# Performance work log

Hardware: AMD Instinct MI355X
Metric: run time of the kernel (lower is better)

Reference implementation:

```python
import jax, jax.numpy as jnp
import numpy as np

B, L, D_SEQ, D_GLOBAL = 32, 2048, 1024, 1024
H, DK, DV = 16, 64, 64


def setup_inputs() -> dict:
    key = jax.random.key(0)
    k1, k2, k3, k4, k5 = jax.random.split(key, 5)
    scale = 0.05
    return {
        "X": jax.random.normal(k1, (B, D_GLOBAL), dtype=jnp.float32),
        "S": jax.random.normal(k2, (B, L, D_SEQ), dtype=jnp.float32),
        "Wq": jax.random.normal(k3, (H, D_GLOBAL, DK), dtype=jnp.float32) * scale,
        "Wk": jax.random.normal(k4, (H, D_SEQ, DK), dtype=jnp.float32) * scale,
        "Wv": jax.random.normal(k5, (H, D_SEQ, DV), dtype=jnp.float32) * scale,
    }


def reference(X, S, Wq, Wk, Wv):
    # X: [B, d_global], S: [B, L, d_seq]
    d_key = Wq.shape[-1]
    inv_sqrt_dk = 1.0 / jnp.sqrt(jnp.float32(d_key))
    # Values: gelu (exact, erf-based like tf default) projection -> [B, H, L, DV]
    VS = jax.nn.gelu(jnp.einsum("bld,hdv->bhlv", S, Wv), approximate=False)
    # Single global query per head: tanh projection -> [B, H, DK]
    Q = jnp.tanh(jnp.einsum("bd,hdk->bhk", X, Wq))
    # Keys: tanh projection -> [B, H, L, DK]
    KS = jnp.tanh(jnp.einsum("bld,hdk->bhlk", S, Wk))
    # Attention logits (batched GEMV): [B, H, L]
    logits = jnp.einsum("bhk,bhlk->bhl", Q, KS) * inv_sqrt_dk
    Z = jax.nn.softmax(logits, axis=-1)
    # Weighted sum of values: [B, H, DV] -> flatten to [B, H*DV]
    Y = jnp.einsum("bhl,bhlv->bhv", Z, VS)
    return Y.reshape(Y.shape[0], -1)
```

## Files before the change

### kernel.cpp

```cpp
#include <hip/hip_runtime.h>
#include <math.h>

#define B_   32
#define L_   2048
#define DSEQ 1024
#define DGLB 1024
#define H_   16
#define DK_  64
#define DV_  64
#define LT   64
#define NT   (L_/LT)
#define PSTRIDE 66

#define WC_KSTRIDE 4096
#define WC_HSTRIDE 131072

#define AS1 __attribute__((address_space(1)))
#define AS3 __attribute__((address_space(3)))

using u16    = unsigned short;
using bf16x8 = __attribute__((ext_vector_type(8))) short;
using f32x4  = __attribute__((ext_vector_type(4))) float;

__device__ __forceinline__ u16 f2bf(float x) {
  union { float f; unsigned int u; } v; v.f = x;
  return (u16)((v.u + 0x7fffu + ((v.u >> 16) & 1u)) >> 16);
}

__device__ __forceinline__ float tanh_fast(float x) {
  float e = __builtin_exp2f(x * 2.885390081777927f);
  return 1.f - 2.f/(e + 1.f);
}

__device__ __forceinline__ float erf_fast(float x) {
  float ax = fabsf(x);
  float t  = 1.f/(1.f + 0.3275911f*ax);
  float p  = t*(0.254829592f + t*(-0.284496736f + t*(1.421413741f +
             t*(-1.453152027f + t*1.061405429f))));
  float e  = __builtin_exp2f(-ax*ax*1.4426950408889634f);
  float r  = 1.f - p*e;
  return copysignf(r, x);
}

#define PHASE_BARRIER(N)                                   \
  do {                                                     \
    __builtin_amdgcn_sched_barrier(0);                     \
    asm volatile("s_waitcnt vmcnt(" #N ")" ::: "memory");  \
    __builtin_amdgcn_s_barrier();                          \
    __builtin_amdgcn_sched_barrier(0);                     \
  } while (0)

__global__ void pack_w_kernel(const float* __restrict__ Wk,
                              const float* __restrict__ Wv,
                              u16* __restrict__ Wc) {
  const int h = blockIdx.x, j = blockIdx.y;
  const float* src = (j < DK_) ? (Wk + (size_t)h*DSEQ*DK_ + j)
                               : (Wv + (size_t)h*DSEQ*DV_ + (j - DK_));
  u16* dst = Wc + (size_t)h*WC_HSTRIDE + (size_t)j*32;
  for (int d = threadIdx.x; d < DSEQ; d += blockDim.x)
    dst[(size_t)(d >> 5)*WC_KSTRIDE + (d & 31)] = f2bf(src[(size_t)d*64]);
}

__global__ void s2bf_kernel(const float* __restrict__ S, u16* __restrict__ Sb) {
  const size_t G = (size_t)B_*L_*DSEQ/8;
  for (size_t i = (size_t)blockIdx.x*256 + threadIdx.x; i < G; i += (size_t)4096*256) {
    const float4* sp = (const float4*)(S + i*8);
    float4 v0 = sp[0], v1 = sp[1];
    bf16x8 wv;
    wv[0]=(short)f2bf(v0.x); wv[1]=(short)f2bf(v0.y);
    wv[2]=(short)f2bf(v0.z); wv[3]=(short)f2bf(v0.w);
    wv[4]=(short)f2bf(v1.x); wv[5]=(short)f2bf(v1.y);
    wv[6]=(short)f2bf(v1.z); wv[7]=(short)f2bf(v1.w);
    *(bf16x8*)(Sb + i*8) = wv;
  }
}

__global__ void q_proj_kernel(const float* __restrict__ X,
                              const float* __restrict__ Wq,
                              float* __restrict__ Q) {
  const int h = blockIdx.x, b0 = blockIdx.y*4, k = threadIdx.x;
  const float* w = Wq + (size_t)h*DGLB*DK_ + k;
  float a0=0.f, a1=0.f, a2=0.f, a3=0.f;
  for (int d = 0; d < DGLB; ++d) {
    float wv = w[(size_t)d*DK_];
    a0 += X[(size_t)(b0+0)*DGLB + d]*wv;
    a1 += X[(size_t)(b0+1)*DGLB + d]*wv;
    a2 += X[(size_t)(b0+2)*DGLB + d]*wv;
    a3 += X[(size_t)(b0+3)*DGLB + d]*wv;
  }
  Q[((size_t)(b0+0)*H_+h)*DK_+k] = tanhf(a0);
  Q[((size_t)(b0+1)*H_+h)*DK_+k] = tanhf(a1);
  Q[((size_t)(b0+2)*H_+h)*DK_+k] = tanhf(a2);
  Q[((size_t)(b0+3)*H_+h)*DK_+k] = tanhf(a3);
}

template<int BF16SRC>
__global__ __launch_bounds__(256, 3) void fused_kernel(
    const float* __restrict__ S, const u16* __restrict__ Sb,
    const u16* __restrict__ Wc, const float* __restrict__ Q,
    float* __restrict__ part) {
  __shared__ u16   Slds[3*64*128];
  __shared__ float lpart[2][64];

  const int id   = blockIdx.x;
  const int slot = id & 7;
  const int m    = id >> 3;
  const int tile = (m + (slot << 7)) & 1023;
  const int t    = tile & (NT-1), b = tile >> 5;

  const int tid  = threadIdx.x;
  const int wave = tid >> 6, lane = tid & 63;
  const int lhi  = lane >> 4, llo = lane & 15;
  const int isV  = wave & 1,  hp  = wave >> 1;
  const int h    = slot*2 + hp;

  const u16* wb = Wc + (size_t)h*WC_HSTRIDE + (size_t)(isV*64 + llo)*32 + lhi*8;
  int arow[4];
  #pragma unroll
  for (int rt = 0; rt < 4; ++rt) arow[rt] = (rt*16 + llo)*256;

  const u16*   Sv = Sb + ((size_t)b*L_ + (size_t)t*LT)*DSEQ;
  const float* Sf = S  + ((size_t)b*L_ + (size_t)t*LT)*DSEQ;

  auto stage_gl = [&](int sub) {
    const int bs = (sub % 3) * 8192;
    #pragma unroll
    for (int it = 0; it < 4; ++it) {
      const int j   = wave*4 + it;
      const int row = 4*j + (lane >> 4);
      const int g   = (lane & 15) ^ (row & 15);
      const u16* gp = Sv + (size_t)row*DSEQ + sub*128 + (g << 3);
      __builtin_amdgcn_global_load_lds(
          (const AS1 void*)gp, (AS3 void*)(Slds + bs + j*512), 16, 0, 0);
    }
  };
  auto stage_reg = [&](int sub) {
    const int bs = (sub % 3) * 16384;
    #pragma unroll
    for (int it = 0; it < 4; ++it) {
      int f = it*256 + tid, row = f >> 4, q = f & 15;
      int g = q ^ (row & 15);
      const float4* sp = (const float4*)(Sf + (size_t)row*DSEQ + sub*128 + g*8);
      float4 v0 = sp[0], v1 = sp[1];
      bf16x8 wv;
      wv[0]=(short)f2bf(v0.x); wv[1]=(short)f2bf(v0.y);
      wv[2]=(short)f2bf(v0.z); wv[3]=(short)f2bf(v0.w);
      wv[4]=(short)f2bf(v1.x); wv[5]=(short)f2bf(v1.y);
      wv[6]=(short)f2bf(v1.z); wv[7]=(short)f2bf(v1.w);
      *(bf16x8*)((char*)Slds + bs + row*256 + q*16) = wv;
    }
  };

  f32x4 acc[4][4];
  #pragma unroll
  for (int rt = 0; rt < 4; ++rt)
    #pragma unroll
    for (int c = 0; c < 4; ++c) acc[rt][c] = {0.f,0.f,0.f,0.f};

  if (BF16SRC) {
    stage_gl(0);
    stage_gl(1);
    __builtin_amdgcn_sched_barrier(0);
  }
  bf16x8 bA[4], bB[4], bC[4], bD[4];
  #pragma unroll
  for (int c = 0; c < 4; ++c) bA[c] = *(const bf16x8*)(wb + (size_t)0*WC_KSTRIDE + c*512);
  #pragma unroll
  for (int c = 0; c < 4; ++c) bB[c] = *(const bf16x8*)(wb + (size_t)1*WC_KSTRIDE + c*512);
  #pragma unroll
  for (int c = 0; c < 4; ++c) bC[c] = *(const bf16x8*)(wb + (size_t)2*WC_KSTRIDE + c*512);
  #pragma unroll
  for (int c = 0; c < 4; ++c) bD[c] = *(const bf16x8*)(wb + (size_t)3*WC_KSTRIDE + c*512);
  const u16* wbp = wb + (size_t)4*WC_KSTRIDE;
  if (BF16SRC) PHASE_BARRIER(20);

#define KSTEP(BUF, kk)                                                        \
  do {                                                                        \
    const int colb = (((kk)*4 + lhi) ^ llo) << 4;                             \
    __builtin_amdgcn_s_setprio(1);                                            \
    _Pragma("unroll")                                                         \
    for (int rt = 0; rt < 4; ++rt) {                                          \
      bf16x8 af = *(const bf16x8*)(cb + arow[rt] + colb);                     \
      acc[rt][0] = __builtin_amdgcn_mfma_f32_16x16x32_bf16(af, BUF[0], acc[rt][0], 0,0,0); \
      acc[rt][1] = __builtin_amdgcn_mfma_f32_16x16x32_bf16(af, BUF[1], acc[rt][1], 0,0,0); \
      acc[rt][2] = __builtin_amdgcn_mfma_f32_16x16x32_bf16(af, BUF[2], acc[rt][2], 0,0,0); \
      acc[rt][3] = __builtin_amdgcn_mfma_f32_16x16x32_bf16(af, BUF[3], acc[rt][3], 0,0,0); \
    }                                                                         \
    __builtin_amdgcn_s_setprio(0);                                            \
    _Pragma("unroll")                                                         \
    for (int c = 0; c < 4; ++c)                                               \
      BUF[c] = *(const bf16x8*)(wbp + c*512);                                 \
    wbp += ((s*4 + (kk) + 4) == 31) ? -(ptrdiff_t)(31*WC_KSTRIDE)             \
                                    : (ptrdiff_t)WC_KSTRIDE;                  \
  } while (0)

  #pragma unroll
  for (int s = 0; s < 8; ++s) {
    if (BF16SRC) {
      if (s < 6) { stage_gl(s + 2); __builtin_amdgcn_sched_barrier(0); }
    } else {
      stage_reg(s);
      __syncthreads();
    }
    const char* cb = (const char*)Slds + (s % 3)*16384;
    KSTEP(bA, 0); KSTEP(bB, 1); KSTEP(bC, 2); KSTEP(bD, 3);
    if (BF16SRC) {
      if (s < 6)       PHASE_BARRIER(36);
      else if (s == 6) PHASE_BARRIER(32);
    } else {
      __syncthreads();
    }
  }
#undef KSTEP

  if (!isV) {
    const float* Qb = Q + ((size_t)b*H_ + h)*DK_;
    float q[4];
    #pragma unroll
    for (int c = 0; c < 4; ++c) q[c] = Qb[16*c + llo];
    #pragma unroll
    for (int rt = 0; rt < 4; ++rt) {
      #pragma unroll
      for (int r = 0; r < 4; ++r) {
        float pl = q[0]*tanh_fast(acc[rt][0][r]) + q[1]*tanh_fast(acc[rt][1][r])
                 + q[2]*tanh_fast(acc[rt][2][r]) + q[3]*tanh_fast(acc[rt][3][r]);
        pl += __shfl_xor(pl, 1); pl += __shfl_xor(pl, 2);
        pl += __shfl_xor(pl, 4); pl += __shfl_xor(pl, 8);
        if (llo == 0) lpart[hp][rt*16 + lhi*4 + r] = pl;
      }
    }
  } else {
    #pragma unroll
    for (int rt = 0; rt < 4; ++rt)
      #pragma unroll
      for (int c = 0; c < 4; ++c)
        #pragma unroll
        for (int r = 0; r < 4; ++r) {
          float x = acc[rt][c][r];
          acc[rt][c][r] = 0.5f*x*(1.f + erf_fast(x*0.70710678118654752f));
        }
  }
  __syncthreads();

  if (isV) {
    float lg = lpart[hp][lane] * 0.125f;
    float mx = lg;
    #pragma unroll
    for (int mk = 1; mk < 64; mk <<= 1) mx = fmaxf(mx, __shfl_xor(mx, mk));
    float ev = __expf(lg - mx);
    float sv = ev;
    #pragma unroll
    for (int mk = 1; mk < 64; mk <<= 1) sv += __shfl_xor(sv, mk);

    float er[16];
    #pragma unroll
    for (int rt = 0; rt < 4; ++rt)
      #pragma unroll
      for (int r = 0; r < 4; ++r)
        er[rt*4 + r] = __shfl(ev, rt*16 + lhi*4 + r);

    float* pt = part + (((size_t)b*H_ + h)*NT + t)*PSTRIDE;
    #pragma unroll
    for (int c = 0; c < 4; ++c) {
      float y = 0.f;
      #pragma unroll
      for (int rt = 0; rt < 4; ++rt)
        #pragma unroll
        for (int r = 0; r < 4; ++r)
          y += er[rt*4 + r]*acc[rt][c][r];
      y += __shfl_xor(y, 16); y += __shfl_xor(y, 32);
      if (lhi == 0) pt[2 + 16*c + llo] = y;
    }
    if (lane == 0) { pt[0] = mx; pt[1] = sv; }
  }
}

__global__ void finalize_kernel(const float* __restrict__ part,
                                float* __restrict__ out) {
  const int h = blockIdx.x, b = blockIdx.y, v = threadIdx.x;
  const float* p = part + ((size_t)b*H_ + h)*(size_t)NT*PSTRIDE;
  float M = -3.0e38f;
  for (int tt = 0; tt < NT; ++tt) M = fmaxf(M, p[tt*PSTRIDE]);
  float ss = 0.f, y = 0.f;
  for (int tt = 0; tt < NT; ++tt) {
    float w = expf(p[tt*PSTRIDE] - M);
    ss += w*p[tt*PSTRIDE + 1];
    y  += w*p[tt*PSTRIDE + 2 + v];
  }
  out[((size_t)b*H_ + h)*DV_ + v] = y/ss;
}

extern "C" void kernel_launch(void* const* d_in, const int* in_sizes, int n_in,
                              void* d_out, int out_size, void* d_ws, size_t ws_size,
                              hipStream_t stream) {
  const float* X  = (const float*)d_in[0];
  const float* S  = (const float*)d_in[1];
  const float* Wq = (const float*)d_in[2];
  const float* Wk = (const float*)d_in[3];
  const float* Wv = (const float*)d_in[4];
  float* out = (float*)d_out;

  char* ws = (char*)d_ws;
  u16*   Wc    = (u16*)ws;
  float* Qbuf  = (float*)(ws + (4u<<20));
  float* part  = (float*)(ws + (4u<<20) + (128u<<10));
  u16*   Sb    = (u16*)(ws + (16u<<20));
  const bool useBf = ws_size >= (144ull << 20);

  pack_w_kernel  <<<dim3(H_, 128),  256, 0, stream>>>(Wk, Wv, Wc);
  q_proj_kernel  <<<dim3(H_, B_/4),  64, 0, stream>>>(X, Wq, Qbuf);
  if (useBf) {
    s2bf_kernel         <<<dim3(4096), 256, 0, stream>>>(S, Sb);
    fused_kernel<1>     <<<dim3(NT*B_*8), 256, 0, stream>>>(S, Sb, Wc, Qbuf, part);
  } else {
    fused_kernel<0>     <<<dim3(NT*B_*8), 256, 0, stream>>>(S, Sb, Wc, Qbuf, part);
  }
  finalize_kernel<<<dim3(H_, B_),    64, 0, stream>>>(part, out);
}
```

Before: 460.8 us.

## Remap fused-kernel blocks per XCD for L2 reuse and split Q projection reduction

The fused kernel's block-to-(tile, head-pair) mapping is rewritten so that each XCD works on only two head pairs and half the tiles. This is meant to raise L2 reuse of the packed weights and the S tiles inside each XCD. The Q projection now uses 256 threads that split the reduction dimension four ways and combine the partial sums through shared memory, which cuts the serial loop length. The stage offset also gains a mask, and many loop variables are renamed to avoid shadowing the new 'c' variable.

```diff
diff --git a/kernel.cpp b/kernel.cpp
--- a/kernel.cpp
+++ b/kernel.cpp
@@ -78,20 +78,27 @@
 __global__ void q_proj_kernel(const float* __restrict__ X,
                               const float* __restrict__ Wq,
                               float* __restrict__ Q) {
-  const int h = blockIdx.x, b0 = blockIdx.y*4, k = threadIdx.x;
-  const float* w = Wq + (size_t)h*DGLB*DK_ + k;
+  __shared__ float red[4][4][64];
+  const int h = blockIdx.x, b0 = blockIdx.y*4;
+  const int k = threadIdx.x & 63, dd = threadIdx.x >> 6;
+  const float* w = Wq + (size_t)h*DGLB*DK_ + (size_t)dd*256*DK_ + k;
   float a0=0.f, a1=0.f, a2=0.f, a3=0.f;
-  for (int d = 0; d < DGLB; ++d) {
+  for (int d = 0; d < 256; ++d) {
     float wv = w[(size_t)d*DK_];
-    a0 += X[(size_t)(b0+0)*DGLB + d]*wv;
-    a1 += X[(size_t)(b0+1)*DGLB + d]*wv;
-    a2 += X[(size_t)(b0+2)*DGLB + d]*wv;
-    a3 += X[(size_t)(b0+3)*DGLB + d]*wv;
-  }
-  Q[((size_t)(b0+0)*H_+h)*DK_+k] = tanhf(a0);
-  Q[((size_t)(b0+1)*H_+h)*DK_+k] = tanhf(a1);
-  Q[((size_t)(b0+2)*H_+h)*DK_+k] = tanhf(a2);
-  Q[((size_t)(b0+3)*H_+h)*DK_+k] = tanhf(a3);
+    a0 += X[(size_t)(b0+0)*DGLB + dd*256 + d]*wv;
+    a1 += X[(size_t)(b0+1)*DGLB + dd*256 + d]*wv;
+    a2 += X[(size_t)(b0+2)*DGLB + dd*256 + d]*wv;
+    a3 += X[(size_t)(b0+3)*DGLB + dd*256 + d]*wv;
+  }
+  red[dd][0][k]=a0; red[dd][1][k]=a1; red[dd][2][k]=a2; red[dd][3][k]=a3;
+  __syncthreads();
+  if (dd == 0) {
+    #pragma unroll
+    for (int bb = 0; bb < 4; ++bb) {
+      float s = red[0][bb][k]+red[1][bb][k]+red[2][bb][k]+red[3][bb][k];
+      Q[((size_t)(b0+bb)*H_+h)*DK_+k] = tanhf(s);
+    }
+  }
 }
 
 template<int BF16SRC>
@@ -103,16 +110,21 @@
   __shared__ float lpart[2][64];
 
   const int id   = blockIdx.x;
-  const int slot = id & 7;
-  const int m    = id >> 3;
-  const int tile = (m + (slot << 7)) & 1023;
+  const int xcd  = id & 7;
+  const int j    = xcd >> 1;
+  const int c    = xcd & 1;
+  const int idx  = id >> 3;
+  const int psel = idx & 1;
+  const int mm   = idx >> 1;
+  const int pair = 2*j + psel;
+  const int tile = (((mm + (j << 7)) & 511) << 1) | c;
   const int t    = tile & (NT-1), b = tile >> 5;
 
   const int tid  = threadIdx.x;
   const int wave = tid >> 6, lane = tid & 63;
   const int lhi  = lane >> 4, llo = lane & 15;
   const int isV  = wave & 1,  hp  = wave >> 1;
-  const int h    = slot*2 + hp;
+  const int h    = pair*2 + hp;
 
   const u16* wb = Wc + (size_t)h*WC_HSTRIDE + (size_t)(isV*64 + llo)*32 + lhi*8;
   int arow[4];
@@ -124,23 +136,25 @@
 
   auto stage_gl = [&](int sub) {
     const int bs = (sub % 3) * 8192;
+    const int ko = (sub & 7) * 128;
     #pragma unroll
     for (int it = 0; it < 4; ++it) {
-      const int j   = wave*4 + it;
-      const int row = 4*j + (lane >> 4);
+      const int jj  = wave*4 + it;
+      const int row = 4*jj + (lane >> 4);
       const int g   = (lane & 15) ^ (row & 15);
-      const u16* gp = Sv + (size_t)row*DSEQ + sub*128 + (g << 3);
+      const u16* gp = Sv + (size_t)row*DSEQ + ko + (g << 3);
       __builtin_amdgcn_global_load_lds(
-          (const AS1 void*)gp, (AS3 void*)(Slds + bs + j*512), 16, 0, 0);
+          (const AS1 void*)gp, (AS3 void*)(Slds + bs + jj*512), 16, 0, 0);
     }
   };
   auto stage_reg = [&](int sub) {
     const int bs = (sub % 3) * 16384;
+    const int ko = (sub & 7) * 128;
     #pragma unroll
     for (int it = 0; it < 4; ++it) {
       int f = it*256 + tid, row = f >> 4, q = f & 15;
       int g = q ^ (row & 15);
-      const float4* sp = (const float4*)(Sf + (size_t)row*DSEQ + sub*128 + g*8);
+      const float4* sp = (const float4*)(Sf + (size_t)row*DSEQ + ko + g*8);
       float4 v0 = sp[0], v1 = sp[1];
       bf16x8 wv;
       wv[0]=(short)f2bf(v0.x); wv[1]=(short)f2bf(v0.y);
@@ -155,7 +169,7 @@
   #pragma unroll
   for (int rt = 0; rt < 4; ++rt)
     #pragma unroll
-    for (int c = 0; c < 4; ++c) acc[rt][c] = {0.f,0.f,0.f,0.f};
+    for (int cc = 0; cc < 4; ++cc) acc[rt][cc] = {0.f,0.f,0.f,0.f};
 
   if (BF16SRC) {
     stage_gl(0);
@@ -164,13 +178,13 @@
   }
   bf16x8 bA[4], bB[4], bC[4], bD[4];
   #pragma unroll
-  for (int c = 0; c < 4; ++c) bA[c] = *(const bf16x8*)(wb + (size_t)0*WC_KSTRIDE + c*512);
-  #pragma unroll
-  for (int c = 0; c < 4; ++c) bB[c] = *(const bf16x8*)(wb + (size_t)1*WC_KSTRIDE + c*512);
-  #pragma unroll
-  for (int c = 0; c < 4; ++c) bC[c] = *(const bf16x8*)(wb + (size_t)2*WC_KSTRIDE + c*512);
-  #pragma unroll
-  for (int c = 0; c < 4; ++c) bD[c] = *(const bf16x8*)(wb + (size_t)3*WC_KSTRIDE + c*512);
+  for (int cc = 0; cc < 4; ++cc) bA[cc] = *(const bf16x8*)(wb + (size_t)0*WC_KSTRIDE + cc*512);
+  #pragma unroll
+  for (int cc = 0; cc < 4; ++cc) bB[cc] = *(const bf16x8*)(wb + (size_t)1*WC_KSTRIDE + cc*512);
+  #pragma unroll
+  for (int cc = 0; cc < 4; ++cc) bC[cc] = *(const bf16x8*)(wb + (size_t)2*WC_KSTRIDE + cc*512);
+  #pragma unroll
+  for (int cc = 0; cc < 4; ++cc) bD[cc] = *(const bf16x8*)(wb + (size_t)3*WC_KSTRIDE + cc*512);
   const u16* wbp = wb + (size_t)4*WC_KSTRIDE;
   if (BF16SRC) PHASE_BARRIER(20);
 
@@ -187,11 +201,13 @@
       acc[rt][3] = __builtin_amdgcn_mfma_f32_16x16x32_bf16(af, BUF[3], acc[rt][3], 0,0,0); \
     }                                                                         \
     __builtin_amdgcn_s_setprio(0);                                            \
-    _Pragma("unroll")                                                         \
-    for (int c = 0; c < 4; ++c)                                               \
-      BUF[c] = *(const bf16x8*)(wbp + c*512);                                 \
-    wbp += ((s*4 + (kk) + 4) == 31) ? -(ptrdiff_t)(31*WC_KSTRIDE)             \
-                                    : (ptrdiff_t)WC_KSTRIDE;                  \
+    {                                                                         \
+      _Pragma("unroll")                                                       \
+      for (int cc = 0; cc < 4; ++cc)                                          \
+        BUF[cc] = *(const bf16x8*)(wbp + cc*512);                             \
+      wbp += ((s*4 + (kk) + 4) == 31) ? -(ptrdiff_t)(31*WC_KSTRIDE)           \
+                                      : (ptrdiff_t)WC_KSTRIDE;                \
+    }                                                                         \
   } while (0)
 
   #pragma unroll
@@ -217,7 +233,7 @@
     const float* Qb = Q + ((size_t)b*H_ + h)*DK_;
     float q[4];
     #pragma unroll
-    for (int c = 0; c < 4; ++c) q[c] = Qb[16*c + llo];
+    for (int cc = 0; cc < 4; ++cc) q[cc] = Qb[16*cc + llo];
     #pragma unroll
     for (int rt = 0; rt < 4; ++rt) {
       #pragma unroll
@@ -233,11 +249,11 @@
     #pragma unroll
     for (int rt = 0; rt < 4; ++rt)
       #pragma unroll
-      for (int c = 0; c < 4; ++c)
+      for (int cc = 0; cc < 4; ++cc)
         #pragma unroll
         for (int r = 0; r < 4; ++r) {
-          float x = acc[rt][c][r];
-          acc[rt][c][r] = 0.5f*x*(1.f + erf_fast(x*0.70710678118654752f));
+          float x = acc[rt][cc][r];
+          acc[rt][cc][r] = 0.5f*x*(1.f + erf_fast(x*0.70710678118654752f));
         }
   }
   __syncthreads();
@@ -261,15 +277,15 @@
 
     float* pt = part + (((size_t)b*H_ + h)*NT + t)*PSTRIDE;
     #pragma unroll
-    for (int c = 0; c < 4; ++c) {
+    for (int cc = 0; cc < 4; ++cc) {
       float y = 0.f;
       #pragma unroll
       for (int rt = 0; rt < 4; ++rt)
         #pragma unroll
         for (int r = 0; r < 4; ++r)
-          y += er[rt*4 + r]*acc[rt][c][r];
+          y += er[rt*4 + r]*acc[rt][cc][r];
       y += __shfl_xor(y, 16); y += __shfl_xor(y, 32);
-      if (lhi == 0) pt[2 + 16*c + llo] = y;
+      if (lhi == 0) pt[2 + 16*cc + llo] = y;
     }
     if (lane == 0) { pt[0] = mx; pt[1] = sv; }
   }
@@ -308,12 +324,12 @@
   const bool useBf = ws_size >= (144ull << 20);
 
   pack_w_kernel  <<<dim3(H_, 128),  256, 0, stream>>>(Wk, Wv, Wc);
-  q_proj_kernel  <<<dim3(H_, B_/4),  64, 0, stream>>>(X, Wq, Qbuf);
+  q_proj_kernel  <<<dim3(H_, B_/4), 256, 0, stream>>>(X, Wq, Qbuf);
   if (useBf) {
-    s2bf_kernel         <<<dim3(4096), 256, 0, stream>>>(S, Sb);
-    fused_kernel<1>     <<<dim3(NT*B_*8), 256, 0, stream>>>(S, Sb, Wc, Qbuf, part);
+    s2bf_kernel       <<<dim3(4096), 256, 0, stream>>>(S, Sb);
+    fused_kernel<1>   <<<dim3(8192), 256, 0, stream>>>(S, Sb, Wc, Qbuf, part);
   } else {
-    fused_kernel<0>     <<<dim3(NT*B_*8), 256, 0, stream>>>(S, Sb, Wc, Qbuf, part);
+    fused_kernel<0>   <<<dim3(8192), 256, 0, stream>>>(S, Sb, Wc, Qbuf, part);
   }
   finalize_kernel<<<dim3(H_, B_),    64, 0, stream>>>(part, out);
 }
```

After: 418.4 us. 1.1x faster.
